# Kernel tuning notes

Hardware: AMD Instinct MI355X
Metric: run time of the kernel (lower is better)

## Reference

```python
import jax, jax.numpy as jnp
import numpy as np

B, T, DIM = 2, 2048, 2048
H, HKV, HD = 16, 4, 128
ROPE_BASE = 10000.0
RMS_EPS = 1.1920929e-07  # torch F.rms_norm default eps = finfo(fp32).eps


def setup_inputs() -> dict:
    key = jax.random.key(0)
    ks = jax.random.split(key, 5)
    s = DIM ** -0.5
    return {
        "x": jax.random.normal(ks[0], (B, T, DIM), jnp.float32),
        "Wq": jax.random.normal(ks[1], (DIM, DIM), jnp.float32) * s,
        "Wk": jax.random.normal(ks[2], (DIM, HKV * HD), jnp.float32) * s,
        "Wv": jax.random.normal(ks[3], (DIM, HKV * HD), jnp.float32) * s,
        "Wo": jax.random.normal(ks[4], (DIM, DIM), jnp.float32) * s,
        "q_gain": jnp.ones((H,), jnp.float32),
    }


def _rms_norm(x):
    return x * jax.lax.rsqrt(jnp.mean(x * x, axis=-1, keepdims=True) + RMS_EPS)


def _rotary(t, hd, base, dtype):
    inv_freq = base ** (-jnp.arange(0, hd, 2, dtype=jnp.float32) / hd)  # [hd/2]
    ang = jnp.arange(t, dtype=jnp.float32)[:, None] * inv_freq[None, :]  # [T, hd/2]
    return jnp.cos(ang).astype(dtype), jnp.sin(ang).astype(dtype)


def _apply_rope(x, cos, sin):
    # x: [B, h, T, D]; cos/sin: [T, D/2] broadcast over batch/heads
    d = x.shape[-1] // 2
    x1, x2 = x[..., :d], x[..., d:]
    return jnp.concatenate([x1 * cos + x2 * sin, -x1 * sin + x2 * cos], axis=-1)


def reference(x, Wq, Wk, Wv, Wo, q_gain):
    Bq, Tq, _ = x.shape
    q = (x @ Wq).reshape(Bq, Tq, H, HD).transpose(0, 2, 1, 3)      # [B,H,T,D]
    k = (x @ Wk).reshape(Bq, Tq, HKV, HD).transpose(0, 2, 1, 3)    # [B,Hkv,T,D]
    v = (x @ Wv).reshape(Bq, Tq, HKV, HD).transpose(0, 2, 1, 3)    # [B,Hkv,T,D]
    q = _rms_norm(q)
    k = _rms_norm(k)
    cos, sin = _rotary(Tq, HD, ROPE_BASE, q.dtype)
    q = _apply_rope(q, cos, sin)
    k = _apply_rope(k, cos, sin)
    q = q * q_gain.astype(q.dtype)[None, :, None, None]
    g = H // HKV
    qg = q.reshape(Bq, HKV, g, Tq, HD)
    # causal GQA SDPA
    scores = jnp.einsum('bkgqd,bkld->bkgql', qg, k) * (HD ** -0.5)
    causal = jnp.tril(jnp.ones((Tq, Tq), bool))
    scores = jnp.where(causal, scores, -jnp.inf)
    p = jax.nn.softmax(scores, axis=-1)
    yg = jnp.einsum('bkgql,bkld->bkgqd', p, v)                      # [B,Hkv,g,T,D]
    # XSA: remove component of each output along the token's own value vector
    vn = v / jnp.clip(jnp.linalg.norm(v, axis=-1, keepdims=True), 1e-12)
    vn = vn[:, :, None]                                             # [B,Hkv,1,T,D]
    proj = jnp.sum(yg * vn, axis=-1, keepdims=True) * vn
    y = (yg - proj).reshape(Bq, H, Tq, HD)
    y = y.transpose(0, 2, 1, 3).reshape(Bq, Tq, DIM)
    return y @ Wo
```

## Files before the change

kernel.cpp:

```cpp
#include <hip/hip_runtime.h>

constexpr int SL  = 2048;
constexpr int NB  = 2;
constexpr int NKV = 4;
constexpr int NH  = 16;
constexpr int DM  = 2048;

typedef unsigned short u16;
typedef unsigned int   u32;
typedef short s16x8 __attribute__((ext_vector_type(8)));
typedef float f32x4 __attribute__((ext_vector_type(4)));

__device__ inline u16 f2bf(float x) {
  union { float f; u32 u; } c; c.f = x;
  u32 r = c.u + 0x7fffu + ((c.u >> 16) & 1u);
  return (u16)(r >> 16);
}
__device__ inline float bf2f(u16 h) {
  union { u32 u; float f; } c; c.u = ((u32)h) << 16; return c.f;
}
__device__ inline u32 cvtpk_bf16(float lo, float hi) {
  u32 r;
  asm("v_cvt_pk_bf16_f32 %0, %1, %2" : "=v"(r) : "v"(lo), "v"(hi));
  return r;
}

__device__ inline void gload16(const void* g, void* l) {
  __builtin_amdgcn_global_load_lds((const __attribute__((address_space(1))) void*)g,
                                   (__attribute__((address_space(3))) void*)l, 16, 0, 0);
}

__global__ __launch_bounds__(256) void prep(const float* __restrict__ x,
                                            const float* __restrict__ Wq,
                                            const float* __restrict__ Wk,
                                            const float* __restrict__ Wv,
                                            const float* __restrict__ Wo,
                                            u16* __restrict__ xb,
                                            u16* __restrict__ WT,
                                            u16* __restrict__ WoT) {
  __shared__ float ld[64][65];
  int id = blockIdx.x;
  if (id < 4096) {
    long i = ((long)id * 256 + threadIdx.x) * 8;
    float4 a = *(const float4*)(x + i);
    float4 b = *(const float4*)(x + i + 4);
    uint4 ov;
    ov.x = (u32)f2bf(a.x) | ((u32)f2bf(a.y) << 16);
    ov.y = (u32)f2bf(a.z) | ((u32)f2bf(a.w) << 16);
    ov.z = (u32)f2bf(b.x) | ((u32)f2bf(b.y) << 16);
    ov.w = (u32)f2bf(b.z) | ((u32)f2bf(b.w) << 16);
    *(uint4*)(xb + i) = ov;
    return;
  }
  id -= 4096;
  const float* src; u16* dst; int N; long bx, by;
  const int K = 2048;
  if (id < 1024)      { src = Wq; dst = WT;                         N = 2048; bx = id & 31; by = id >> 5; }
  else if (id < 1280) { int j = id - 1024; src = Wk; dst = WT + (size_t)2048 * 2048; N = 512; bx = j & 7; by = j >> 3; }
  else if (id < 1536) { int j = id - 1280; src = Wv; dst = WT + (size_t)2560 * 2048; N = 512; bx = j & 7; by = j >> 3; }
  else                { int j = id - 1536; src = Wo; dst = WoT;                     N = 2048; bx = j & 31; by = j >> 5; }
  int tid = threadIdx.x;
  long c0 = bx * 64, r0 = by * 64;
#pragma unroll
  for (int i = 0; i < 4; ++i) {
    int e = tid + 256 * i;
    int r = e >> 4, cg = e & 15;
    float4 v = *(const float4*)(src + (r0 + r) * N + c0 + cg * 4);
    ld[r][cg * 4 + 0] = v.x;
    ld[r][cg * 4 + 1] = v.y;
    ld[r][cg * 4 + 2] = v.z;
    ld[r][cg * 4 + 3] = v.w;
  }
  __syncthreads();
#pragma unroll
  for (int i = 0; i < 4; ++i) {
    int e = tid + 256 * i;
    int cg = e & 15, rr = e >> 4;
    ushort4 o;
    o.x = f2bf(ld[cg * 4 + 0][rr]);
    o.y = f2bf(ld[cg * 4 + 1][rr]);
    o.z = f2bf(ld[cg * 4 + 2][rr]);
    o.w = f2bf(ld[cg * 4 + 3][rr]);
    *(ushort4*)(dst + (c0 + rr) * K + r0 + cg * 4) = o;
  }
}

template <int BF16OUT>
__global__ __launch_bounds__(256, 2) void gemm_bt(const u16* __restrict__ A,
                                                  const u16* __restrict__ BT,
                                                  float* __restrict__ Cf,
                                                  u16* __restrict__ Cb,
                                                  int M, int N, int K) {
  __shared__ __align__(16) char As[256 * 128];
  __shared__ __align__(16) char Bs[128 * 128];
  const int tid = threadIdx.x;
  const int lane = tid & 63;
  const int w = tid >> 6;
  const int wm = w >> 1, wn = w & 1;
  const int lr = lane & 15, lg = lane >> 4;

  const int flat = blockIdx.y * gridDim.x + blockIdx.x;
  const int chunk = (gridDim.x * gridDim.y) >> 3;
  const int nidx = (flat & 7) * chunk + (flat >> 3);
  const int bxl = nidx / gridDim.y;
  const int byl = nidx % gridDim.y;
  const long bm = (long)bxl * 256;
  const long bn = (long)byl * 128;

  f32x4 acc[8][4] = {};

  const int nt = K >> 6;
#pragma unroll 1
  for (int ti = 0; ti < nt; ++ti) {
    const int kt0 = ti << 6;
#pragma unroll
    for (int i = 0; i < 8; ++i) {
      int c = tid + 256 * i;
      int row = c >> 3;
      int slot = (c & 7) << 4;
      int gs = slot ^ ((row & 7) << 4);
      gload16(A + (bm + row) * K + kt0 + (gs >> 1), As + c * 16);
    }
#pragma unroll
    for (int i = 0; i < 4; ++i) {
      int c = tid + 256 * i;
      int row = c >> 3;
      int slot = (c & 7) << 4;
      int gs = slot ^ ((row & 7) << 4);
      gload16(BT + (bn + row) * K + kt0 + (gs >> 1), Bs + c * 16);
    }
    __syncthreads();

    __builtin_amdgcn_s_setprio(1);
#pragma unroll
    for (int kk = 0; kk < 2; ++kk) {
      int colB = (kk * 32 + lg * 8) * 2;
      s16x8 af[8], bfv[4];
#pragma unroll
      for (int m = 0; m < 8; ++m) {
        int row = wm * 128 + m * 16 + lr;
        af[m] = *(const s16x8*)(As + row * 128 + (colB ^ ((row & 7) << 4)));
      }
#pragma unroll
      for (int n = 0; n < 4; ++n) {
        int row = wn * 64 + n * 16 + lr;
        bfv[n] = *(const s16x8*)(Bs + row * 128 + (colB ^ ((row & 7) << 4)));
      }
#pragma unroll
      for (int m = 0; m < 8; ++m)
#pragma unroll
        for (int n = 0; n < 4; ++n)
          acc[m][n] = __builtin_amdgcn_mfma_f32_16x16x32_bf16(af[m], bfv[n], acc[m][n], 0, 0, 0);
    }
    __builtin_amdgcn_s_setprio(0);
    __syncthreads();
  }

#pragma unroll
  for (int m = 0; m < 8; ++m)
#pragma unroll
    for (int n = 0; n < 4; ++n) {
      long row = bm + wm * 128 + m * 16 + lg * 4;
      long col = bn + wn * 64 + n * 16 + lr;
#pragma unroll
      for (int r = 0; r < 4; ++r) {
        if (BF16OUT)
          Cb[(row + r) * N + col] = f2bf(acc[m][n][r]);
        else
          Cf[(row + r) * N + col] = acc[m][n][r];
      }
    }
}

__global__ __launch_bounds__(256) void postqkv(const u16* __restrict__ qkv,
                                               const float* __restrict__ qg,
                                               u16* __restrict__ qb, u16* __restrict__ kb,
                                               u16* __restrict__ vt) {
  __shared__ u16 ldt[64][136];
  int id = blockIdx.x;
  int tid = threadIdx.x;
  if (id < 4096) {
    int token = id;
    int b = token >> 11, t = token & (SL - 1);
    int lane = tid & 63, w = tid >> 6;
    const u16* row = qkv + (long)token * 3072;
    float inv = __expf(-(float)lane * (9.210340371976184f / 64.0f));
    float ang = (float)t * inv;
    float c = cosf(ang), s = sinf(ang);
    for (int slot = w; slot < 20; slot += 4) {
      const u16* p = row + slot * 128;
      float v0 = bf2f(p[lane]), v1 = bf2f(p[lane + 64]);
      float ss = v0 * v0 + v1 * v1;
      for (int m = 1; m < 64; m <<= 1) ss += __shfl_xor(ss, m);
      float rms = rsqrtf(ss * (1.0f / 128.0f) + 1.1920929e-07f);
      v0 *= rms; v1 *= rms;
      float o0 =  v0 * c + v1 * s;
      float o1 = -v0 * s + v1 * c;
      u16* dst;
      if (slot < 16) {
        float g = qg[slot] * 0.08838834764831845f * 1.4426950408889634f;
        o0 *= g; o1 *= g;
        dst = qb + ((long)(b * NH + slot) * SL + t) * 128;
      } else {
        dst = kb + ((long)(b * NKV + (slot - 16)) * SL + t) * 128;
      }
      dst[lane] = f2bf(o0);
      dst[lane + 64] = f2bf(o1);
    }
    return;
  }
  int blk = id - 4096;
  int tt = blk & 31, kvb = blk >> 5;
  const u16* src = qkv + (long)(((kvb >> 2) * SL) + tt * 64) * 3072 + 2560 + (kvb & 3) * 128;
#pragma unroll
  for (int i = 0; i < 4; ++i) {
    int e = tid + 256 * i;
    int r = e >> 4, dg = e & 15;
    uint4 v = *(const uint4*)(src + (long)r * 3072 + dg * 8);
    *(uint4*)(&ldt[r][dg * 8]) = v;
  }
  __syncthreads();
  u16* dst = vt + (long)kvb * 128 * SL + tt * 64;
#pragma unroll
  for (int i = 0; i < 8; ++i) {
    int e = tid + 256 * i;
    int rg = e & 15, d = e >> 4;
    ushort4 o;
    o.x = ldt[rg * 4 + 0][d];
    o.y = ldt[rg * 4 + 1][d];
    o.z = ldt[rg * 4 + 2][d];
    o.w = ldt[rg * 4 + 3][d];
    *(ushort4*)(dst + (long)d * SL + rg * 4) = o;
  }
}

__global__ __launch_bounds__(256) void attn(const u16* __restrict__ qb, const u16* __restrict__ kb,
                                            const u16* __restrict__ vt, const float* __restrict__ qg,
                                            const u16* __restrict__ qkvb, u16* __restrict__ yb) {
  __shared__ __align__(16) char Ks[2][64 * 256];
  __shared__ __align__(16) char Vs[2][128 * 128];
  __shared__ __align__(16) char Ps[64 * 128];
  const int tid = threadIdx.x, lane = tid & 63, w = tid >> 6;

  const int flat = blockIdx.y * 16 + blockIdx.x;
  const int nidx = (flat & 7) * 64 + (flat >> 3);
  const int pairIdx = nidx & 15;
  const int bh = nidx >> 4;

  const int b = bh >> 4, h = bh & 15;
  const int kvh = h >> 2;
  const int lr = lane & 15, lg = lane >> 4;

  const float Ms = 16.3223f * fabsf(qg[h]);

  const u16* kbase = kb + (long)(b * NKV + kvh) * SL * 128;
  const u16* vbase = vt + (long)(b * NKV + kvh) * 128 * SL;

#pragma unroll 1
  for (int pass = 0; pass < 2; ++pass) {
    const int qblk = pass ? 31 - pairIdx : pairIdx;
    const int ntile = qblk + 1;

    const u16* qp = qb + ((long)bh * SL + qblk * 64 + w * 16 + lr) * 128;
    s16x8 qf[4];
#pragma unroll
    for (int kk = 0; kk < 4; ++kk) qf[kk] = *(const s16x8*)(qp + kk * 32 + lg * 8);

    f32x4 acc[8] = {};
    float lsum[4] = {0.f, 0.f, 0.f, 0.f};

#pragma unroll
    for (int i = 0; i < 4; ++i) {
      int c = tid + 256 * i;
      int row = c >> 4, slot = (c & 15) << 4;
      gload16(kbase + (long)row * 128 + ((slot ^ ((row & 15) << 4)) >> 1), Ks[0] + c * 16);
    }
#pragma unroll
    for (int i = 0; i < 4; ++i) {
      int c = tid + 256 * i;
      int row = c >> 3, slot = (c & 7) << 4;
      gload16(vbase + (long)row * SL + ((slot ^ ((row & 7) << 4)) >> 1), Vs[0] + c * 16);
    }

#pragma unroll 1
    for (int kt = 0; kt < ntile; ++kt) {
      const int cur = kt & 1;
      if (kt + 1 < ntile) {
        const int nx = cur ^ 1;
#pragma unroll
        for (int i = 0; i < 4; ++i) {
          int c = tid + 256 * i;
          int row = c >> 4, slot = (c & 15) << 4;
          gload16(kbase + (long)((kt + 1) * 64 + row) * 128 + ((slot ^ ((row & 15) << 4)) >> 1),
                  Ks[nx] + c * 16);
        }
#pragma unroll
        for (int i = 0; i < 4; ++i) {
          int c = tid + 256 * i;
          int row = c >> 3, slot = (c & 7) << 4;
          gload16(vbase + (long)row * SL + (kt + 1) * 64 + ((slot ^ ((row & 7) << 4)) >> 1),
                  Vs[nx] + c * 16);
        }
        asm volatile("s_waitcnt vmcnt(8)" ::: "memory");
      } else {
        asm volatile("s_waitcnt vmcnt(0)" ::: "memory");
      }
      __builtin_amdgcn_s_barrier();

      f32x4 sv[4];
      __builtin_amdgcn_s_setprio(1);
#pragma unroll
      for (int n = 0; n < 4; ++n) {
        f32x4 z = {0.f, 0.f, 0.f, 0.f};
#pragma unroll
        for (int kk = 0; kk < 4; ++kk) {
          int row = n * 16 + lr;
          s16x8 kf = *(const s16x8*)(Ks[cur] + row * 256 + (((kk * 32 + lg * 8) * 2) ^ ((row & 15) << 4)));
          z = __builtin_amdgcn_mfma_f32_16x16x32_bf16(qf[kk], kf, z, 0, 0, 0);
        }
        sv[n] = z;
      }
      __builtin_amdgcn_s_setprio(0);

      if (kt == qblk) {
#pragma unroll
        for (int n = 0; n < 4; ++n)
#pragma unroll
          for (int r = 0; r < 4; ++r) {
            int colA = n * 16 + lr;
            int rowA = w * 16 + lg * 4 + r;
            if (colA > rowA) sv[n][r] = -1e30f;
          }
      }
#pragma unroll
      for (int n = 0; n < 4; ++n)
#pragma unroll
        for (int r = 0; r < 4; ++r) {
          float p = __builtin_amdgcn_exp2f(sv[n][r] - Ms);
          sv[n][r] = p;
          lsum[r] += p;
        }
#pragma unroll
      for (int n = 0; n < 4; ++n) {
        u32 pk0 = cvtpk_bf16(sv[n][0], sv[n][1]);
        u32 pk1 = cvtpk_bf16(sv[n][2], sv[n][3]);
        int row = w * 16 + lg * 4;
        int colB = (n * 16 + lr) * 2;
        *(u16*)(Ps + (row + 0) * 128 + (colB ^ (((row + 0) & 7) << 4))) = (u16)pk0;
        *(u16*)(Ps + (row + 1) * 128 + (colB ^ (((row + 1) & 7) << 4))) = (u16)(pk0 >> 16);
        *(u16*)(Ps + (row + 2) * 128 + (colB ^ (((row + 2) & 7) << 4))) = (u16)pk1;
        *(u16*)(Ps + (row + 3) * 128 + (colB ^ (((row + 3) & 7) << 4))) = (u16)(pk1 >> 16);
      }
      __builtin_amdgcn_s_setprio(1);
#pragma unroll
      for (int kk = 0; kk < 2; ++kk) {
        int prow = w * 16 + lr;
        s16x8 pa = *(const s16x8*)(Ps + prow * 128 + (((kk * 32 + lg * 8) * 2) ^ ((prow & 7) << 4)));
#pragma unroll
        for (int n = 0; n < 8; ++n) {
          int vrow = n * 16 + lr;
          s16x8 vf = *(const s16x8*)(Vs[cur] + vrow * 128 + (((kk * 32 + lg * 8) * 2) ^ ((vrow & 7) << 4)));
          acc[n] = __builtin_amdgcn_mfma_f32_16x16x32_bf16(pa, vf, acc[n], 0, 0, 0);
        }
      }
      __builtin_amdgcn_s_setprio(0);
      __builtin_amdgcn_s_barrier();
    }

    float inv_l[4];
#pragma unroll
    for (int r = 0; r < 4; ++r) {
      float v = lsum[r];
      v += __shfl_xor(v, 1);
      v += __shfl_xor(v, 2);
      v += __shfl_xor(v, 4);
      v += __shfl_xor(v, 8);
      inv_l[r] = 1.0f / v;
    }
    const int row0 = qblk * 64 + w * 16 + lg * 4;
    float vv[8][4];
    float ssq[4], dot[4];
#pragma unroll
    for (int r = 0; r < 4; ++r) {
      const u16* pr = qkvb + ((long)(b * SL + row0 + r) * 3072) + 2560 + kvh * 128;
      float sq = 0.f;
#pragma unroll
      for (int n = 0; n < 8; ++n) {
        float t = bf2f(pr[n * 16 + lr]);
        vv[n][r] = t;
        sq += t * t;
      }
      ssq[r] = sq;
    }
#pragma unroll
    for (int r = 0; r < 4; ++r) {
      float sq = ssq[r];
      sq += __shfl_xor(sq, 1);
      sq += __shfl_xor(sq, 2);
      sq += __shfl_xor(sq, 4);
      sq += __shfl_xor(sq, 8);
      ssq[r] = sq;
      float d = 0.f;
#pragma unroll
      for (int n = 0; n < 8; ++n) {
        float yn = acc[n][r] * inv_l[r];
        acc[n][r] = yn;
        d += yn * vv[n][r];
      }
      dot[r] = d;
    }
#pragma unroll
    for (int r = 0; r < 4; ++r) {
      float d = dot[r];
      d += __shfl_xor(d, 1);
      d += __shfl_xor(d, 2);
      d += __shfl_xor(d, 4);
      d += __shfl_xor(d, 8);
      dot[r] = d / fmaxf(ssq[r], 1e-24f);
    }
    u16* yp = yb + ((long)(b * SL + row0)) * DM + h * 128;
#pragma unroll
    for (int n = 0; n < 8; ++n)
#pragma unroll
      for (int r = 0; r < 4; ++r)
        yp[(long)r * DM + n * 16 + lr] = f2bf(acc[n][r] - dot[r] * vv[n][r]);
  }
}

extern "C" void kernel_launch(void* const* d_in, const int* in_sizes, int n_in,
                              void* d_out, int out_size, void* d_ws, size_t ws_size,
                              hipStream_t stream) {
  const float* x  = (const float*)d_in[0];
  const float* Wq = (const float*)d_in[1];
  const float* Wk = (const float*)d_in[2];
  const float* Wv = (const float*)d_in[3];
  const float* Wo = (const float*)d_in[4];
  const float* qg = (const float*)d_in[5];
  float* out = (float*)d_out;

  char* p = (char*)d_ws;
  u16* xb    = (u16*)p;   p += (size_t)4096 * 2048 * 2;
  u16* WT    = (u16*)p;   p += (size_t)3072 * 2048 * 2;
  u16* WoT   = (u16*)p;   p += (size_t)2048 * 2048 * 2;
  u16* qkvb  = (u16*)p;   p += (size_t)4096 * 3072 * 2;
  u16* qbuf  = (u16*)p;   p += (size_t)NB * NH * SL * 128 * 2;
  u16* kbuf  = (u16*)p;   p += (size_t)NB * NKV * SL * 128 * 2;
  u16* vtb   = (u16*)p;   p += (size_t)NB * NKV * 128 * SL * 2;
  u16* yb = xb;

  prep<<<6656, 256, 0, stream>>>(x, Wq, Wk, Wv, Wo, xb, WT, WoT);
  gemm_bt<1><<<dim3(16, 24), 256, 0, stream>>>(xb, WT, nullptr, qkvb, 4096, 3072, 2048);
  postqkv<<<4352, 256, 0, stream>>>(qkvb, qg, qbuf, kbuf, vtb);
  attn<<<dim3(16, 32), 256, 0, stream>>>(qbuf, kbuf, vtb, qg, qkvb, yb);
  gemm_bt<0><<<dim3(16, 16), 256, 0, stream>>>(yb, WoT, out, nullptr, 4096, 2048, 2048);
}
```

Before: 202.3 us.

## Use 256x256-tile 8-wave pipelined GEMM for QKV projection

Adds a new QKV projection GEMM that uses 512 threads, 256x256 output tiles and double-buffered LDS. Global loads are split into quarter-tile stages and issued between four MFMA sub-phases, with vmcnt waits and barriers between them. The larger tile raises arithmetic intensity and overlaps loads with compute. It cuts the grid to 192 blocks on a GPU with many CUs, which may underfill the device, and 128KB of LDS may limit residency to one block per CU.

```diff
diff --git a/kernel.cpp b/kernel.cpp
--- a/kernel.cpp
+++ b/kernel.cpp
@@ -85,11 +85,143 @@
   }
 }
 
-template <int BF16OUT>
+__global__ __launch_bounds__(512, 2) void gemm8p(const u16* __restrict__ A,
+                                                 const u16* __restrict__ BT,
+                                                 u16* __restrict__ Cb,
+                                                 int M, int N, int K) {
+  __shared__ __align__(16) char As[2][256 * 128];
+  __shared__ __align__(16) char Bs[2][256 * 128];
+  const int tid = threadIdx.x;
+  const int lane = tid & 63;
+  const int wid = tid >> 6;
+  const int wm = wid >> 2, wn = wid & 3;
+  const int lr = lane & 15, lg = lane >> 4;
+
+  const int flat = blockIdx.y * gridDim.x + blockIdx.x;
+  const int chunk = (gridDim.x * gridDim.y) >> 3;
+  const int nidx = (flat & 7) * chunk + (flat >> 3);
+  const long bm = (long)(nidx / gridDim.y) * 256;
+  const long bn = (long)(nidx % gridDim.y) * 256;
+
+  f32x4 acc[8][4] = {};
+  const int nt = K >> 6;
+
+  auto stage_half = [&](int h) {
+    const int t = h >> 2, ty = h & 3, slot = t & 1;
+    const int kt0 = t << 6;
+    const int rofs = (ty & 1) << 7;
+    const u16* src = (ty < 2) ? (A + (bm + rofs) * (long)K) : (BT + (bn + rofs) * (long)K);
+    char* dst = ((ty < 2) ? As[slot] : Bs[slot]) + (rofs << 7);
+#pragma unroll
+    for (int i = 0; i < 2; ++i) {
+      int c = tid + 512 * i;
+      int row = c >> 3;
+      int slotcol = (c & 7) << 4;
+      int gs = slotcol ^ ((row & 7) << 4);
+      gload16(src + (long)row * K + kt0 + (gs >> 1), dst + c * 16);
+    }
+  };
+
+  for (int h = 0; h < 5; ++h) stage_half(h);
+
+#pragma unroll 1
+  for (int t = 0; t < nt; ++t) {
+    const int S = t & 1;
+    const int hb = 4 * t + 5;
+    const int hmax = 4 * nt;
+    s16x8 af[4][2], bf[2][2];
+
+    auto rdA = [&](int m, int kk) -> s16x8 {
+      int row = wm * 128 + m * 16 + lr;
+      int col = (kk * 32 + lg * 8) * 2;
+      return *(const s16x8*)(As[S] + row * 128 + (col ^ ((row & 7) << 4)));
+    };
+    auto rdB = [&](int n, int kk) -> s16x8 {
+      int row = wn * 64 + n * 16 + lr;
+      int col = (kk * 32 + lg * 8) * 2;
+      return *(const s16x8*)(Bs[S] + row * 128 + (col ^ ((row & 7) << 4)));
+    };
+
+    if (hb < hmax) stage_half(hb);
+    if (t + 1 < nt) asm volatile("s_waitcnt vmcnt(4)" ::: "memory");
+    else            asm volatile("s_waitcnt vmcnt(0)" ::: "memory");
+    __builtin_amdgcn_s_barrier();
+#pragma unroll
+    for (int m = 0; m < 4; ++m) { af[m][0] = rdA(m, 0); af[m][1] = rdA(m, 1); }
+#pragma unroll
+    for (int n = 0; n < 2; ++n) { bf[n][0] = rdB(n, 0); bf[n][1] = rdB(n, 1); }
+    __builtin_amdgcn_s_setprio(1);
+#pragma unroll
+    for (int kk = 0; kk < 2; ++kk)
+#pragma unroll
+      for (int m = 0; m < 4; ++m)
+#pragma unroll
+        for (int n = 0; n < 2; ++n)
+          acc[m][n] = __builtin_amdgcn_mfma_f32_16x16x32_bf16(af[m][kk], bf[n][kk], acc[m][n], 0, 0, 0);
+    __builtin_amdgcn_s_setprio(0);
+    __builtin_amdgcn_s_barrier();
+
+    if (hb + 1 < hmax) stage_half(hb + 1);
+#pragma unroll
+    for (int n = 0; n < 2; ++n) { bf[n][0] = rdB(n + 2, 0); bf[n][1] = rdB(n + 2, 1); }
+    __builtin_amdgcn_s_barrier();
+    __builtin_amdgcn_s_setprio(1);
+#pragma unroll
+    for (int kk = 0; kk < 2; ++kk)
+#pragma unroll
+      for (int m = 0; m < 4; ++m)
+#pragma unroll
+        for (int n = 0; n < 2; ++n)
+          acc[m][n + 2] = __builtin_amdgcn_mfma_f32_16x16x32_bf16(af[m][kk], bf[n][kk], acc[m][n + 2], 0, 0, 0);
+    __builtin_amdgcn_s_setprio(0);
+    __builtin_amdgcn_s_barrier();
+
+    if (hb + 2 < hmax) stage_half(hb + 2);
+#pragma unroll
+    for (int m = 0; m < 4; ++m) { af[m][0] = rdA(m + 4, 0); af[m][1] = rdA(m + 4, 1); }
+    __builtin_amdgcn_s_barrier();
+    __builtin_amdgcn_s_setprio(1);
+#pragma unroll
+    for (int kk = 0; kk < 2; ++kk)
+#pragma unroll
+      for (int m = 0; m < 4; ++m)
+#pragma unroll
+        for (int n = 0; n < 2; ++n)
+          acc[m + 4][n + 2] = __builtin_amdgcn_mfma_f32_16x16x32_bf16(af[m][kk], bf[n][kk], acc[m + 4][n + 2], 0, 0, 0);
+    __builtin_amdgcn_s_setprio(0);
+    __builtin_amdgcn_s_barrier();
+
+    if (hb + 3 < hmax) stage_half(hb + 3);
+#pragma unroll
+    for (int n = 0; n < 2; ++n) { bf[n][0] = rdB(n, 0); bf[n][1] = rdB(n, 1); }
+    __builtin_amdgcn_s_barrier();
+    __builtin_amdgcn_s_setprio(1);
+#pragma unroll
+    for (int kk = 0; kk < 2; ++kk)
+#pragma unroll
+      for (int m = 0; m < 4; ++m)
+#pragma unroll
+        for (int n = 0; n < 2; ++n)
+          acc[m + 4][n] = __builtin_amdgcn_mfma_f32_16x16x32_bf16(af[m][kk], bf[n][kk], acc[m + 4][n], 0, 0, 0);
+    __builtin_amdgcn_s_setprio(0);
+    __builtin_amdgcn_s_barrier();
+  }
+
+#pragma unroll
+  for (int m = 0; m < 8; ++m)
+#pragma unroll
+    for (int n = 0; n < 4; ++n) {
+      long row = bm + wm * 128 + m * 16 + lg * 4;
+      long col = bn + wn * 64 + n * 16 + lr;
+#pragma unroll
+      for (int r = 0; r < 4; ++r)
+        Cb[(row + r) * N + col] = f2bf(acc[m][n][r]);
+    }
+}
+
 __global__ __launch_bounds__(256, 2) void gemm_bt(const u16* __restrict__ A,
                                                   const u16* __restrict__ BT,
                                                   float* __restrict__ Cf,
-                                                  u16* __restrict__ Cb,
                                                   int M, int N, int K) {
   __shared__ __align__(16) char As[256 * 128];
   __shared__ __align__(16) char Bs[128 * 128];
@@ -163,12 +295,8 @@
       long row = bm + wm * 128 + m * 16 + lg * 4;
       long col = bn + wn * 64 + n * 16 + lr;
 #pragma unroll
-      for (int r = 0; r < 4; ++r) {
-        if (BF16OUT)
-          Cb[(row + r) * N + col] = f2bf(acc[m][n][r]);
-        else
-          Cf[(row + r) * N + col] = acc[m][n][r];
-      }
+      for (int r = 0; r < 4; ++r)
+        Cf[(row + r) * N + col] = acc[m][n][r];
     }
 }
 
@@ -449,8 +577,8 @@
   u16* yb = xb;
 
   prep<<<6656, 256, 0, stream>>>(x, Wq, Wk, Wv, Wo, xb, WT, WoT);
-  gemm_bt<1><<<dim3(16, 24), 256, 0, stream>>>(xb, WT, nullptr, qkvb, 4096, 3072, 2048);
+  gemm8p<<<dim3(16, 12), 512, 0, stream>>>(xb, WT, qkvb, 4096, 3072, 2048);
   postqkv<<<4352, 256, 0, stream>>>(qkvb, qg, qbuf, kbuf, vtb);
   attn<<<dim3(16, 32), 256, 0, stream>>>(qbuf, kbuf, vtb, qg, qkvb, yb);
-  gemm_bt<0><<<dim3(16, 16), 256, 0, stream>>>(yb, WoT, out, nullptr, 4096, 2048, 2048);
-}
+  gemm_bt<<<dim3(16, 16), 256, 0, stream>>>(yb, WoT, out, 4096, 2048, 2048);
+}
```

Measured after the change: 236.5 us. +16.9%, slower.
